# Kernel tuning notes

Measured on AMD Instinct MI355X. Metric: run time of the kernel, lower is better.

The kernel has to match this reference:

```python
import jax, jax.numpy as jnp
import numpy as np

FEATURES = 4096
BATCH = 2048


def setup_inputs() -> dict:
    key = jax.random.key(0)
    kx, kk = jax.random.split(key)
    x = jax.random.normal(kx, (BATCH, FEATURES), dtype=jnp.float32)
    kernel = jax.random.normal(kk, (FEATURES,), dtype=jnp.float32)
    return {"x": x, "kernel": kernel}


def reference(x, kernel):
    n = kernel.shape[0]
    i = jnp.arange(n)[:, None]   # [n,1]
    j = jnp.arange(n)[None, :]   # [1,n]
    idx = i - j                   # Toeplitz offsets
    # W[i,j] = kernel[i-j] if i>=j else 0  (causal lower-triangular Toeplitz)
    W = jnp.where(idx >= 0, kernel[jnp.clip(idx, 0, n - 1)], 0.0)
    # out[b,i] = sum_{j<=i} x[b,j] * kernel[i-j]  == x @ W.T
    return x @ W.T
```

## Files before the change

### kernel.cpp

```cpp
#include <hip/hip_runtime.h>
#include <hip/hip_bf16.h>


typedef unsigned short u16;
typedef __attribute__((ext_vector_type(8))) short  bf16x8;
typedef __attribute__((ext_vector_type(8))) unsigned short u16x8;
typedef __attribute__((ext_vector_type(4))) float  f32x4;

#define KDIM 4096
#define NDIM 4096
#define MDIM 2048
#define KREV_STRIDE 4608
#define KREV_BYTES  (8 * KREV_STRIDE * 2)

#define MFMA_BF16 __builtin_amdgcn_mfma_f32_16x16x32_bf16

static __device__ inline u16 f2bf(float f) {
  unsigned u = __builtin_bit_cast(unsigned, f);
  unsigned r = u + 0x7FFFu + ((u >> 16) & 1u);
  return (u16)(r >> 16);
}

static __device__ inline void async_copy16(const void* g, void* l) {
  __builtin_amdgcn_global_load_lds((const __attribute__((address_space(1))) void*)g,
                                   (__attribute__((address_space(3))) void*)l,
                                   16, 0, 0);
}

__global__ __launch_bounds__(256) void prep(const float* __restrict__ x,
                                            const float* __restrict__ kern,
                                            u16* __restrict__ xb,
                                            u16* __restrict__ krevs,
                                            int conv_blocks) {
  int kblk = (int)blockIdx.x - conv_blocks;
  if (kblk >= 0) {
    int u = kblk * 256 + threadIdx.x;
    for (int a = 0; a < 8; ++a) {
      int t = u + a - 8;
      u16 v = 0;
      if (t >= 0 && t <= 4095) v = f2bf(kern[4095 - t]);
      krevs[a * KREV_STRIDE + u] = v;
    }
  } else {
    unsigned tg  = blockIdx.x * 256 + threadIdx.x;
    unsigned l   = tg & 63;
    unsigned kb  = (tg >> 6) & 127;
    unsigned rg  = tg >> 13;
    unsigned row = rg * 16 + (l & 15);
    unsigned k   = kb * 32 + (l >> 4) * 8;
    const f32x4* p = (const f32x4*)(x + (size_t)row * KDIM + k);
    f32x4 v0 = p[0], v1 = p[1];
    u16x8 r;
    r[0] = f2bf(v0[0]); r[1] = f2bf(v0[1]); r[2] = f2bf(v0[2]); r[3] = f2bf(v0[3]);
    r[4] = f2bf(v1[0]); r[5] = f2bf(v1[1]); r[6] = f2bf(v1[2]); r[7] = f2bf(v1[3]);
    *(u16x8*)(xb + (size_t)tg * 8) = r;
  }
}

template <bool CONV>
__global__ __launch_bounds__(512, 2) void toeplitz_gemm(const void* __restrict__ Av,
                                                        const u16* __restrict__ krevs,
                                                        float* __restrict__ out) {
  __shared__ __align__(16) char smem_raw[73984];
  u16*   B_all = (u16*)smem_raw;
  f32x4* ep    = (f32x4*)smem_raw;

  const int tid  = threadIdx.x;
  const int w    = tid >> 6;
  const int g    = w >> 2;
  const int wl   = w & 3;
  const int lane = tid & 63;
  const int lane16 = lane & 15;
  const int quad   = lane >> 4;
  const int wm = wl >> 1;
  const int wn = wl & 1;

  const int b   = (int)blockIdx.x;
  const int x_  = b & 7;
  const int jj  = b >> 3;
  const int p_  = x_ + 8 * (jj & 1);
  const int ctp = jj >> 1;
  const int ct1 = 31 - ctp;
  const int ct2 = ctp;
  const int m0  = p_ * 128;

  const int stride1 = 128 * (ct1 + 1) + 200;
  const int stride2 = 128 * (ct2 + 1) + 200;
  const int base2   = 8 * stride1;
  const int W1 = 3968 - 128 * ct1;
  const int W2 = 3968 - 128 * ct2;

  const int wmu = __builtin_amdgcn_readfirstlane(wm);
  const int gu  = __builtin_amdgcn_readfirstlane(g);
  const u16*   xb2 = (const u16*)Av;
  const float* xf  = (const float*)Av;
  int aoffs[4];
  for (int fm = 0; fm < 4; ++fm)
    aoffs[fm] = (p_ * 8 + wmu * 4 + fm) * 65536 + gu * 1024 + lane * 8;
  const int rowb = m0 + wm * 64 + lane16;

  auto ldA = [&](int fm, int t, int kk) -> bf16x8 {
    return *(const bf16x8*)(xb2 + aoffs[fm] + t * 2048 + kk * 512);
  };
  auto ldAc = [&](int fm, int t, int kk) -> bf16x8 {
    const float* px = xf + (size_t)(rowb + fm * 16) * KDIM +
                      t * 128 + gu * 64 + kk * 32 + quad * 8;
    f32x4 v0 = *(const f32x4*)px, v1 = *(const f32x4*)(px + 4);
    u16x8 r;
    r[0]=f2bf(v0[0]); r[1]=f2bf(v0[1]); r[2]=f2bf(v0[2]); r[3]=f2bf(v0[3]);
    r[4]=f2bf(v1[0]); r[5]=f2bf(v1[1]); r[6]=f2bf(v1[2]); r[7]=f2bf(v1[3]);
    return __builtin_bit_cast(bf16x8, r);
  };

  auto stageWin = [&](int base_e, int stride_e, int Wp) {
    const u16* src = krevs + w * KREV_STRIDE + Wp;
    char* dstb = smem_raw + (size_t)(base_e + w * stride_e) * 2;
    for (int c = 0; c * 512 < stride_e; ++c) {
      int idx = c * 512 + lane * 8;
      if (idx < stride_e)
        async_copy16(src + idx, dstb + (size_t)c * 1024);
    }
  };
  stageWin(0, stride1, W1);
  stageWin(base2, stride2, W2);
  asm volatile("s_waitcnt vmcnt(0)" ::: "memory");
  __builtin_amdgcn_s_barrier();
  asm volatile("" ::: "memory");

  auto runPhase = [&](int ctq, int base_e, int stride_q, int Wq) {
    const int n0q = ctq * 128;
    int boff[4];
    for (int fn = 0; fn < 4; ++fn) {
      int n_g = n0q + wn * 64 + fn * 16 + lane16;
      int s0  = 4095 - n_g + quad * 8;
      int a   = s0 & 7;
      boff[fn] = base_e + a * stride_q + (s0 - a + 8 - Wq);
    }
    f32x4 acc[4][4] = {};

    if constexpr (!CONV) {
      bf16x8 afA[4], afB[4], bvA[4], bvB[4];
#pragma unroll
      for (int fm = 0; fm < 4; ++fm) afA[fm] = ldA(fm, 0, 0);
#pragma unroll
      for (int fm = 0; fm < 4; ++fm) afB[fm] = ldA(fm, 0, 1);
#pragma unroll
      for (int fn = 0; fn < 4; ++fn)
        bvA[fn] = *(const bf16x8*)(&B_all[boff[fn] + g * 64]);
      for (int t = 0; ; ++t) {
        const int ks = t * 128 + g * 64;
#pragma unroll
        for (int fn = 0; fn < 4; ++fn)
          bvB[fn] = *(const bf16x8*)(&B_all[boff[fn] + ks + 32]);
#pragma unroll
        for (int fn = 0; fn < 4; ++fn)
#pragma unroll
          for (int fm = 0; fm < 4; ++fm)
            acc[fm][fn] = MFMA_BF16(afA[fm], bvA[fn], acc[fm][fn], 0, 0, 0);
        if (t < ctq)
#pragma unroll
          for (int fm = 0; fm < 4; ++fm) afA[fm] = ldA(fm, t + 1, 0);
        if (t < ctq)
#pragma unroll
          for (int fn = 0; fn < 4; ++fn)
            bvA[fn] = *(const bf16x8*)(&B_all[boff[fn] + ks + 128]);
#pragma unroll
        for (int fn = 0; fn < 4; ++fn)
#pragma unroll
          for (int fm = 0; fm < 4; ++fm)
            acc[fm][fn] = MFMA_BF16(afB[fm], bvB[fn], acc[fm][fn], 0, 0, 0);
        if (t == ctq) break;
#pragma unroll
        for (int fm = 0; fm < 4; ++fm) afB[fm] = ldA(fm, t + 1, 1);
      }
    } else {
      for (int t = 0; t <= ctq; ++t) {
        const int ks = t * 128 + g * 64;
#pragma unroll
        for (int kk = 0; kk < 2; ++kk) {
          bf16x8 af[4];
#pragma unroll
          for (int fm = 0; fm < 4; ++fm) af[fm] = ldAc(fm, t, kk);
#pragma unroll
          for (int fn = 0; fn < 4; ++fn) {
            bf16x8 bv = *(const bf16x8*)(&B_all[boff[fn] + ks + kk * 32]);
#pragma unroll
            for (int fm = 0; fm < 4; ++fm)
              acc[fm][fn] = MFMA_BF16(af[fm], bv, acc[fm][fn], 0, 0, 0);
          }
        }
      }
    }

    const int j = tid & 255;
#pragma unroll
    for (int r = 0; r < 2; ++r) {
      __syncthreads();
      if (g == 1) {
        for (int fm2 = 0; fm2 < 2; ++fm2)
          for (int fn = 0; fn < 4; ++fn)
            ep[j * 9 + fm2 * 4 + fn] = acc[r * 2 + fm2][fn];
      }
      __syncthreads();
      if (g == 0) {
        for (int fm2 = 0; fm2 < 2; ++fm2)
          for (int fn = 0; fn < 4; ++fn) {
            f32x4 v = acc[r * 2 + fm2][fn];
            f32x4 o = ep[j * 9 + fm2 * 4 + fn];
            v[0] += o[0]; v[1] += o[1]; v[2] += o[2]; v[3] += o[3];
            int fm = r * 2 + fm2;
            int row_base = m0 + wm * 64 + fm * 16 + quad * 4;
            int col = n0q + wn * 64 + fn * 16 + lane16;
            for (int rr = 0; rr < 4; ++rr)
              out[(size_t)(row_base + rr) * NDIM + col] = v[rr];
          }
      }
    }
  };

  runPhase(ct1, 0, stride1, W1);
  runPhase(ct2, base2, stride2, W2);
}

extern "C" void kernel_launch(void* const* d_in, const int* in_sizes, int n_in,
                              void* d_out, int out_size, void* d_ws, size_t ws_size,
                              hipStream_t stream) {
  const float* x    = (const float*)d_in[0];
  const float* kern = (const float*)d_in[1];
  float* out = (float*)d_out;

  u16* krevs = (u16*)d_ws;
  u16* xb    = (u16*)((char*)d_ws + KREV_BYTES);
  const size_t need_fast = (size_t)KREV_BYTES + (size_t)MDIM * KDIM * 2;

  if (ws_size >= need_fast) {
    prep<<<4096 + 18, 256, 0, stream>>>(x, kern, xb, krevs, 4096);
    toeplitz_gemm<false><<<256, 512, 0, stream>>>(xb, krevs, out);
  } else {
    prep<<<18, 256, 0, stream>>>(x, kern, xb, krevs, 0);
    toeplitz_gemm<true><<<256, 512, 0, stream>>>(x, krevs, out);
  }
}
```

Before: 114.0 us.

## Fuse fp32-to-bf16 conversion of x into GEMM with register-prefetched loads

Removes the separate prep pass that converted x to a pre-swizzled bf16 buffer in workspace. The GEMM now reads fp32 x directly and converts it in registers, prefetching the next K tile's fp32 values one iteration ahead so the global loads overlap with the MFMAs. This drops one full read and write of x through HBM and one launch's worth of work. In exchange it reads twice as many bytes of A inside the GEMM and needs more registers for the fp32 staging, which may lower occupancy.

```diff
diff --git a/kernel.cpp b/kernel.cpp
--- a/kernel.cpp
+++ b/kernel.cpp
@@ -21,44 +21,31 @@
   return (u16)(r >> 16);
 }
 
+static __device__ inline bf16x8 cvt8(f32x4 a, f32x4 b) {
+  u16x8 r;
+  r[0] = f2bf(a[0]); r[1] = f2bf(a[1]); r[2] = f2bf(a[2]); r[3] = f2bf(a[3]);
+  r[4] = f2bf(b[0]); r[5] = f2bf(b[1]); r[6] = f2bf(b[2]); r[7] = f2bf(b[3]);
+  return __builtin_bit_cast(bf16x8, r);
+}
+
 static __device__ inline void async_copy16(const void* g, void* l) {
   __builtin_amdgcn_global_load_lds((const __attribute__((address_space(1))) void*)g,
                                    (__attribute__((address_space(3))) void*)l,
                                    16, 0, 0);
 }
 
-__global__ __launch_bounds__(256) void prep(const float* __restrict__ x,
-                                            const float* __restrict__ kern,
-                                            u16* __restrict__ xb,
-                                            u16* __restrict__ krevs,
-                                            int conv_blocks) {
-  int kblk = (int)blockIdx.x - conv_blocks;
-  if (kblk >= 0) {
-    int u = kblk * 256 + threadIdx.x;
-    for (int a = 0; a < 8; ++a) {
-      int t = u + a - 8;
-      u16 v = 0;
-      if (t >= 0 && t <= 4095) v = f2bf(kern[4095 - t]);
-      krevs[a * KREV_STRIDE + u] = v;
-    }
-  } else {
-    unsigned tg  = blockIdx.x * 256 + threadIdx.x;
-    unsigned l   = tg & 63;
-    unsigned kb  = (tg >> 6) & 127;
-    unsigned rg  = tg >> 13;
-    unsigned row = rg * 16 + (l & 15);
-    unsigned k   = kb * 32 + (l >> 4) * 8;
-    const f32x4* p = (const f32x4*)(x + (size_t)row * KDIM + k);
-    f32x4 v0 = p[0], v1 = p[1];
-    u16x8 r;
-    r[0] = f2bf(v0[0]); r[1] = f2bf(v0[1]); r[2] = f2bf(v0[2]); r[3] = f2bf(v0[3]);
-    r[4] = f2bf(v1[0]); r[5] = f2bf(v1[1]); r[6] = f2bf(v1[2]); r[7] = f2bf(v1[3]);
-    *(u16x8*)(xb + (size_t)tg * 8) = r;
+__global__ __launch_bounds__(256) void prep(const float* __restrict__ kern,
+                                            u16* __restrict__ krevs) {
+  int u = (int)blockIdx.x * 256 + threadIdx.x;
+  for (int a = 0; a < 8; ++a) {
+    int t = u + a - 8;
+    u16 v = 0;
+    if (t >= 0 && t <= 4095) v = f2bf(kern[4095 - t]);
+    krevs[a * KREV_STRIDE + u] = v;
   }
 }
 
-template <bool CONV>
-__global__ __launch_bounds__(512, 2) void toeplitz_gemm(const void* __restrict__ Av,
+__global__ __launch_bounds__(512, 2) void toeplitz_gemm(const float* __restrict__ x,
                                                         const u16* __restrict__ krevs,
                                                         float* __restrict__ out) {
   __shared__ __align__(16) char smem_raw[73984];
@@ -90,27 +77,11 @@
   const int W1 = 3968 - 128 * ct1;
   const int W2 = 3968 - 128 * ct2;
 
-  const int wmu = __builtin_amdgcn_readfirstlane(wm);
-  const int gu  = __builtin_amdgcn_readfirstlane(g);
-  const u16*   xb2 = (const u16*)Av;
-  const float* xf  = (const float*)Av;
-  int aoffs[4];
+  const int gu = __builtin_amdgcn_readfirstlane(g);
+  const int rowb = m0 + wm * 64 + lane16;
+  const float* pxb[4];
   for (int fm = 0; fm < 4; ++fm)
-    aoffs[fm] = (p_ * 8 + wmu * 4 + fm) * 65536 + gu * 1024 + lane * 8;
-  const int rowb = m0 + wm * 64 + lane16;
-
-  auto ldA = [&](int fm, int t, int kk) -> bf16x8 {
-    return *(const bf16x8*)(xb2 + aoffs[fm] + t * 2048 + kk * 512);
-  };
-  auto ldAc = [&](int fm, int t, int kk) -> bf16x8 {
-    const float* px = xf + (size_t)(rowb + fm * 16) * KDIM +
-                      t * 128 + gu * 64 + kk * 32 + quad * 8;
-    f32x4 v0 = *(const f32x4*)px, v1 = *(const f32x4*)(px + 4);
-    u16x8 r;
-    r[0]=f2bf(v0[0]); r[1]=f2bf(v0[1]); r[2]=f2bf(v0[2]); r[3]=f2bf(v0[3]);
-    r[4]=f2bf(v1[0]); r[5]=f2bf(v1[1]); r[6]=f2bf(v1[2]); r[7]=f2bf(v1[3]);
-    return __builtin_bit_cast(bf16x8, r);
-  };
+    pxb[fm] = x + (size_t)(rowb + fm * 16) * KDIM + gu * 64 + quad * 8;
 
   auto stageWin = [&](int base_e, int stride_e, int Wp) {
     const u16* src = krevs + w * KREV_STRIDE + Wp;
@@ -137,59 +108,57 @@
       boff[fn] = base_e + a * stride_q + (s0 - a + 8 - Wq);
     }
     f32x4 acc[4][4] = {};
-
-    if constexpr (!CONV) {
-      bf16x8 afA[4], afB[4], bvA[4], bvB[4];
-#pragma unroll
-      for (int fm = 0; fm < 4; ++fm) afA[fm] = ldA(fm, 0, 0);
-#pragma unroll
-      for (int fm = 0; fm < 4; ++fm) afB[fm] = ldA(fm, 0, 1);
-#pragma unroll
-      for (int fn = 0; fn < 4; ++fn)
-        bvA[fn] = *(const bf16x8*)(&B_all[boff[fn] + g * 64]);
-      for (int t = 0; ; ++t) {
-        const int ks = t * 128 + g * 64;
-#pragma unroll
-        for (int fn = 0; fn < 4; ++fn)
-          bvB[fn] = *(const bf16x8*)(&B_all[boff[fn] + ks + 32]);
-#pragma unroll
-        for (int fn = 0; fn < 4; ++fn)
-#pragma unroll
-          for (int fm = 0; fm < 4; ++fm)
-            acc[fm][fn] = MFMA_BF16(afA[fm], bvA[fn], acc[fm][fn], 0, 0, 0);
-        if (t < ctq)
-#pragma unroll
-          for (int fm = 0; fm < 4; ++fm) afA[fm] = ldA(fm, t + 1, 0);
-        if (t < ctq)
-#pragma unroll
-          for (int fn = 0; fn < 4; ++fn)
-            bvA[fn] = *(const bf16x8*)(&B_all[boff[fn] + ks + 128]);
-#pragma unroll
-        for (int fn = 0; fn < 4; ++fn)
-#pragma unroll
-          for (int fm = 0; fm < 4; ++fm)
-            acc[fm][fn] = MFMA_BF16(afB[fm], bvB[fn], acc[fm][fn], 0, 0, 0);
-        if (t == ctq) break;
-#pragma unroll
-        for (int fm = 0; fm < 4; ++fm) afB[fm] = ldA(fm, t + 1, 1);
-      }
-    } else {
-      for (int t = 0; t <= ctq; ++t) {
-        const int ks = t * 128 + g * 64;
-#pragma unroll
-        for (int kk = 0; kk < 2; ++kk) {
-          bf16x8 af[4];
-#pragma unroll
-          for (int fm = 0; fm < 4; ++fm) af[fm] = ldAc(fm, t, kk);
-#pragma unroll
-          for (int fn = 0; fn < 4; ++fn) {
-            bf16x8 bv = *(const bf16x8*)(&B_all[boff[fn] + ks + kk * 32]);
-#pragma unroll
-            for (int fm = 0; fm < 4; ++fm)
-              acc[fm][fn] = MFMA_BF16(af[fm], bv, acc[fm][fn], 0, 0, 0);
-          }
+    f32x4 rA[4][2], rB[4][2];
+    bf16x8 afA[4], afB[4], bvA[4], bvB[4];
+
+#pragma unroll
+    for (int fm = 0; fm < 4; ++fm) {
+      const f32x4* p0 = (const f32x4*)(pxb[fm]);
+      rA[fm][0] = p0[0]; rA[fm][1] = p0[1];
+      const f32x4* p1 = (const f32x4*)(pxb[fm] + 32);
+      rB[fm][0] = p1[0]; rB[fm][1] = p1[1];
+    }
+#pragma unroll
+    for (int fm = 0; fm < 4; ++fm) afA[fm] = cvt8(rA[fm][0], rA[fm][1]);
+#pragma unroll
+    for (int fm = 0; fm < 4; ++fm) afB[fm] = cvt8(rB[fm][0], rB[fm][1]);
+#pragma unroll
+    for (int fn = 0; fn < 4; ++fn)
+      bvA[fn] = *(const bf16x8*)(&B_all[boff[fn] + g * 64]);
+
+    for (int t = 0; ; ++t) {
+      const int ks = t * 128 + g * 64;
+      if (t < ctq) {
+#pragma unroll
+        for (int fm = 0; fm < 4; ++fm) {
+          const f32x4* p0 = (const f32x4*)(pxb[fm] + (t + 1) * 128);
+          rA[fm][0] = p0[0]; rA[fm][1] = p0[1];
+          const f32x4* p1 = (const f32x4*)(pxb[fm] + (t + 1) * 128 + 32);
+          rB[fm][0] = p1[0]; rB[fm][1] = p1[1];
         }
       }
+#pragma unroll
+      for (int fn = 0; fn < 4; ++fn)
+        bvB[fn] = *(const bf16x8*)(&B_all[boff[fn] + ks + 32]);
+#pragma unroll
+      for (int fn = 0; fn < 4; ++fn)
+#pragma unroll
+        for (int fm = 0; fm < 4; ++fm)
+          acc[fm][fn] = MFMA_BF16(afA[fm], bvA[fn], acc[fm][fn], 0, 0, 0);
+      if (t < ctq)
+#pragma unroll
+        for (int fn = 0; fn < 4; ++fn)
+          bvA[fn] = *(const bf16x8*)(&B_all[boff[fn] + ks + 128]);
+#pragma unroll
+      for (int fn = 0; fn < 4; ++fn)
+#pragma unroll
+        for (int fm = 0; fm < 4; ++fm)
+          acc[fm][fn] = MFMA_BF16(afB[fm], bvB[fn], acc[fm][fn], 0, 0, 0);
+      if (t == ctq) break;
+#pragma unroll
+      for (int fm = 0; fm < 4; ++fm) afA[fm] = cvt8(rA[fm][0], rA[fm][1]);
+#pragma unroll
+      for (int fm = 0; fm < 4; ++fm) afB[fm] = cvt8(rB[fm][0], rB[fm][1]);
     }
 
     const int j = tid & 255;
@@ -230,14 +199,7 @@
   float* out = (float*)d_out;
 
   u16* krevs = (u16*)d_ws;
-  u16* xb    = (u16*)((char*)d_ws + KREV_BYTES);
-  const size_t need_fast = (size_t)KREV_BYTES + (size_t)MDIM * KDIM * 2;
-
-  if (ws_size >= need_fast) {
-    prep<<<4096 + 18, 256, 0, stream>>>(x, kern, xb, krevs, 4096);
-    toeplitz_gemm<false><<<256, 512, 0, stream>>>(xb, krevs, out);
-  } else {
-    prep<<<18, 256, 0, stream>>>(x, kern, xb, krevs, 0);
-    toeplitz_gemm<true><<<256, 512, 0, stream>>>(x, krevs, out);
-  }
-}
+
+  prep<<<18, 256, 0, stream>>>(kern, krevs);
+  toeplitz_gemm<<<256, 512, 0, stream>>>(x, krevs, out);
+}
```

Result: slower. 199.5 us (+75.1%).
